# Kernel optimization log

Hardware: AMD Instinct MI355X
Metric: run time of the kernel (lower is better)

The kernel has to match this reference:

```python
import jax, jax.numpy as jnp
import numpy as np

B, S, D, H = 2, 2048, 512, 8


def setup_inputs() -> dict:
    key = jax.random.key(0)
    ks = jax.random.split(key, 9)
    scale = 1.0 / np.sqrt(D)
    x = jax.random.normal(ks[0], (B, S, D), dtype=jnp.float32)
    # Per-head full-width projections, stacked over heads: [H, D, D]
    Wq = jax.random.normal(ks[1], (H, D, D), dtype=jnp.float32) * scale
    Wk = jax.random.normal(ks[2], (H, D, D), dtype=jnp.float32) * scale
    Wv = jax.random.normal(ks[3], (H, D, D), dtype=jnp.float32) * scale
    bq = jax.random.normal(ks[4], (H, D), dtype=jnp.float32) * 0.01
    bk = jax.random.normal(ks[5], (H, D), dtype=jnp.float32) * 0.01
    bv = jax.random.normal(ks[6], (H, D), dtype=jnp.float32) * 0.01
    Wo = jax.random.normal(ks[7], (H * D, D), dtype=jnp.float32) * (1.0 / np.sqrt(H * D))
    bo = jax.random.normal(ks[8], (D,), dtype=jnp.float32) * 0.01
    return {"x": x, "Wq": Wq, "bq": bq, "Wk": Wk, "bk": bk, "Wv": Wv, "bv": bv, "Wo": Wo, "bo": bo}


def reference(x, Wq, bq, Wk, bk, Wv, bv, Wo, bo):
    # Batched per-head projections: [B,S,D] x [H,D,E] -> [B,H,S,E]
    q = jnp.einsum('bsd,hde->bhse', x, Wq) + bq[None, :, None, :]
    k = jnp.einsum('bsd,hde->bhse', x, Wk) + bk[None, :, None, :]
    v = jnp.einsum('bsd,hde->bhse', x, Wv) + bv[None, :, None, :]
    # NOTE: original module has NO 1/sqrt(d) scaling
    scores = jnp.einsum('bhse,bhte->bhst', q, k)  # [B,H,S,S]
    attn = jax.nn.softmax(scores, axis=-1)
    out = jnp.einsum('bhst,bhte->bhse', attn, v)  # [B,H,S,D]
    # Concat heads along feature dim: [B,S,H*D]
    cat = out.transpose(0, 2, 1, 3).reshape(B, S, H * D)
    return cat @ Wo + bo
```

## Files before the change

### kernel.cpp

```cpp
#include <hip/hip_runtime.h>

typedef _Float16 f16;
typedef _Float16 f16x8 __attribute__((ext_vector_type(8)));
typedef float f32x4 __attribute__((ext_vector_type(4)));

#define B_ 2
#define S_ 2048
#define D_ 512
#define H_ 8

__device__ inline void async_ld16(const void* g, void* l) {
  __builtin_amdgcn_global_load_lds((__attribute__((address_space(1))) void*)(g),
                                   (__attribute__((address_space(3))) void*)(l),
                                   16, 0, 0);
}

__global__ __launch_bounds__(256) void cvt_f16(const float* __restrict__ src,
                                               f16* __restrict__ dst, long n) {
  long i = (long)blockIdx.x * 256 + threadIdx.x;
  if (i >= n) return;
  dst[i] = (f16)src[i];
}

__global__ __launch_bounds__(256) void transpose_f32(const float* __restrict__ src,
                                                     f16* __restrict__ dst, int R, int C) {
  __shared__ float t[32][33];
  size_t zoff = (size_t)blockIdx.z * R * C;
  const float* s = src + zoff;
  int tx = threadIdx.x;
  int ty = threadIdx.y;
  int c0 = blockIdx.x * 32, r0 = blockIdx.y * 32;
#pragma unroll
  for (int i = 0; i < 4; ++i)
    t[ty + i * 8][tx] = s[(size_t)(r0 + ty + i * 8) * C + c0 + tx];
  __syncthreads();
#pragma unroll
  for (int i = 0; i < 4; ++i)
    dst[zoff + (size_t)(c0 + ty + i * 8) * R + r0 + tx] = (f16)t[tx][ty + i * 8];
}

__global__ __launch_bounds__(256) void reduce_out(const float* __restrict__ part,
                                                  const float* __restrict__ bo,
                                                  float* __restrict__ out, long n, int nslab) {
  long i = (long)blockIdx.x * 256 + threadIdx.x;
  if (i >= n) return;
  float v = bo[i & (D_ - 1)];
  for (int s = 0; s < nslab; ++s) v += part[(long)s * n + i];
  out[i] = v;
}

struct GemmArgs {
  const f16 *A, *Bm;
  void* C;
  const float* bias;
  float* Mloc;
  int K, lda, ldb, ldc;
  int zbase, NG, PBG;
  long sAp, sAb, sAg, sAz;
  long sBp, sBb, sBg, sBz;
  long sCp, sCb, sCg, sCz;
  long sbp, sbb, sbg, sbz;
  long sMlz;
};

template <typename OutT, int BIAS, bool PEXP>
__global__ __launch_bounds__(256) void gemm_nt(GemmArgs p) {
  int zloc = blockIdx.z;
  int zi = p.zbase + zloc;
  int pp = zi / p.PBG; int rz = zi - pp * p.PBG;
  int bb = rz / p.NG;  int g = rz - bb * p.NG;
  const f16* A  = p.A + (pp * p.sAp + bb * p.sAb + g * p.sAg + (long)zloc * p.sAz);
  const f16* Bm = p.Bm + (pp * p.sBp + bb * p.sBb + g * p.sBg + (long)zloc * p.sBz);
  OutT* C = (OutT*)p.C + (pp * p.sCp + bb * p.sCb + g * p.sCg + (long)zloc * p.sCz);
  const float* bias = nullptr;
  if (BIAS) bias = p.bias + (pp * p.sbp + bb * p.sbb + g * p.sbg + (long)zloc * p.sbz);

  __shared__ f16 lA[4096];
  __shared__ f16 lB[4096];
  __shared__ float lMx[PEXP ? 256 : 1];
  __shared__ f16 lR[PEXP ? 32 * 136 : 1];

  int tid = threadIdx.x;
  int lane = tid & 63;
  int w = tid >> 6;
  int wm = (w >> 1) << 6;
  int wn = (w & 1) << 6;
  long bm = (long)blockIdx.y * 128;
  long bn = (long)blockIdx.x * 128;

  f32x4 acc[4][4] = {};
  int qd = lane >> 4;
  int fr = lane & 15;

  int q0 = tid, q1 = tid + 256;
  int r0s = q0 >> 2, c0s = (q0 & 3) ^ ((r0s >> 1) & 3);
  int r1s = q1 >> 2, c1s = (q1 & 3) ^ ((r1s >> 1) & 3);

  for (int k0 = 0; k0 < p.K; k0 += 32) {
    long oa0 = (bm + r0s) * (long)p.lda + (k0 + c0s * 8);
    long oa1 = (bm + r1s) * (long)p.lda + (k0 + c1s * 8);
    long ob0 = (bn + r0s) * (long)p.ldb + (k0 + c0s * 8);
    long ob1 = (bn + r1s) * (long)p.ldb + (k0 + c1s * 8);
    __syncthreads();
    async_ld16(A + oa0,  lA + (size_t)q0 * 8);
    async_ld16(A + oa1,  lA + (size_t)q1 * 8);
    async_ld16(Bm + ob0, lB + (size_t)q0 * 8);
    async_ld16(Bm + ob1, lB + (size_t)q1 * 8);
    __syncthreads();

    f16x8 ah[4], bh[4];
#pragma unroll
    for (int i = 0; i < 4; ++i) {
      int m = wm + i * 16 + fr;
      ah[i] = *(const f16x8*)(lA + ((size_t)m * 4 + (qd ^ ((m >> 1) & 3))) * 8);
      int n = wn + i * 16 + fr;
      bh[i] = *(const f16x8*)(lB + ((size_t)n * 4 + (qd ^ ((n >> 1) & 3))) * 8);
    }
#pragma unroll
    for (int i = 0; i < 4; ++i)
#pragma unroll
      for (int j = 0; j < 4; ++j)
        acc[i][j] = __builtin_amdgcn_mfma_f32_16x16x32_f16(ah[i], bh[j], acc[i][j], 0, 0, 0);
  }

  int rr0 = qd * 4;
  if (PEXP) {
#pragma unroll
    for (int i = 0; i < 4; ++i) {
#pragma unroll
      for (int r = 0; r < 4; ++r) {
        float v = fmaxf(fmaxf(acc[i][0][r], acc[i][1][r]),
                        fmaxf(acc[i][2][r], acc[i][3][r]));
        v = fmaxf(v, __shfl_xor(v, 1, 64));
        v = fmaxf(v, __shfl_xor(v, 2, 64));
        v = fmaxf(v, __shfl_xor(v, 4, 64));
        v = fmaxf(v, __shfl_xor(v, 8, 64));
        if (fr == 0) lMx[(w & 1) * 128 + wm + i * 16 + rr0 + r] = v;
      }
    }
    __syncthreads();
    if (tid < 128) {
      float ml = fmaxf(lMx[tid], lMx[128 + tid]);
      p.Mloc[(long)zloc * p.sMlz + (long)blockIdx.x * S_ + bm + tid] = ml;
    }
    int rowBase = (w >> 1) << 4;
#pragma unroll
    for (int i = 0; i < 4; ++i) {
      __syncthreads();
#pragma unroll
      for (int r = 0; r < 4; ++r) {
        int rl = wm + i * 16 + rr0 + r;
        float ml = fmaxf(lMx[rl], lMx[128 + rl]);
        int rowLoc = rowBase + rr0 + r;
#pragma unroll
        for (int j = 0; j < 4; ++j) {
          int col = wn + j * 16 + fr;
          lR[rowLoc * 136 + col] = (f16)__expf(acc[i][j][r] - ml);
        }
      }
      __syncthreads();
      int rowLoc = tid >> 3;
      int colLoc = (tid & 7) * 16;
      long grow = bm + ((rowLoc & 15) + i * 16) + ((long)(rowLoc >> 4) << 6);
      f16x8 v0 = *(const f16x8*)(lR + rowLoc * 136 + colLoc);
      f16x8 v1 = *(const f16x8*)(lR + rowLoc * 136 + colLoc + 8);
      f16* dst = (f16*)C + grow * (long)p.ldc + bn + colLoc;
      *(f16x8*)(dst) = v0;
      *(f16x8*)(dst + 8) = v1;
    }
  } else {
#pragma unroll
    for (int i = 0; i < 4; ++i) {
#pragma unroll
      for (int j = 0; j < 4; ++j) {
#pragma unroll
        for (int r = 0; r < 4; ++r) {
          long row = bm + wm + i * 16 + rr0 + r;
          long col = bn + wn + j * 16 + fr;
          float v = acc[i][j][r];
          if (BIAS == 1) v += bias[col];
          if (BIAS == 2) v += bias[row];
          C[row * (long)p.ldc + col] = (OutT)v;
        }
      }
    }
  }
}

struct QkvArgs {
  const f16 *xh, *wqk, *wv;
  f16 *qk, *vT;
  const float *bqk, *bv;
};
__global__ __launch_bounds__(256) void qkv_proj(QkvArgs p) {
  const long SD = (long)S_ * D_, DD = (long)D_ * D_, DS = (long)D_ * S_;
  int zi = blockIdx.z;
  int pp = zi >> 4;
  int r = zi & 15;
  int b = r >> 3, h = r & 7;
  int bid = blockIdx.x;
  const f16 *A, *Bm;
  f16* C;
  const float* bias;
  long bm, bn;
  int ldc;
  bool biasRow;
  if (pp < 2) {
    A = p.xh + (long)b * SD;
    Bm = p.wqk + ((long)pp * 8 + h) * DD;
    C = p.qk + (long)zi * SD;
    bias = p.bqk + ((long)pp * 8 + h) * D_;
    bm = (long)(bid >> 2) * 128; bn = (long)(bid & 3) * 128;
    ldc = D_; biasRow = false;
  } else {
    A = p.wv + (long)h * DD;
    Bm = p.xh + (long)b * SD;
    C = p.vT + (long)(b * 8 + h) * DS;
    bias = p.bv + (long)h * D_;
    bm = (long)(bid >> 4) * 128; bn = (long)(bid & 15) * 128;
    ldc = S_; biasRow = true;
  }

  __shared__ f16 lA[4096];
  __shared__ f16 lB[4096];

  int tid = threadIdx.x;
  int lane = tid & 63;
  int w = tid >> 6;
  int wm = (w >> 1) << 6;
  int wn = (w & 1) << 6;

  f32x4 acc[4][4] = {};
  int qd = lane >> 4;
  int fr = lane & 15;

  int q0 = tid, q1 = tid + 256;
  int r0s = q0 >> 2, c0s = (q0 & 3) ^ ((r0s >> 1) & 3);
  int r1s = q1 >> 2, c1s = (q1 & 3) ^ ((r1s >> 1) & 3);

  for (int k0 = 0; k0 < D_; k0 += 32) {
    long oa0 = (bm + r0s) * (long)D_ + (k0 + c0s * 8);
    long oa1 = (bm + r1s) * (long)D_ + (k0 + c1s * 8);
    long ob0 = (bn + r0s) * (long)D_ + (k0 + c0s * 8);
    long ob1 = (bn + r1s) * (long)D_ + (k0 + c1s * 8);
    __syncthreads();
    async_ld16(A + oa0,  lA + (size_t)q0 * 8);
    async_ld16(A + oa1,  lA + (size_t)q1 * 8);
    async_ld16(Bm + ob0, lB + (size_t)q0 * 8);
    async_ld16(Bm + ob1, lB + (size_t)q1 * 8);
    __syncthreads();

    f16x8 ah[4], bh[4];
#pragma unroll
    for (int i = 0; i < 4; ++i) {
      int m = wm + i * 16 + fr;
      ah[i] = *(const f16x8*)(lA + ((size_t)m * 4 + (qd ^ ((m >> 1) & 3))) * 8);
      int n = wn + i * 16 + fr;
      bh[i] = *(const f16x8*)(lB + ((size_t)n * 4 + (qd ^ ((n >> 1) & 3))) * 8);
    }
#pragma unroll
    for (int i = 0; i < 4; ++i)
#pragma unroll
      for (int j = 0; j < 4; ++j)
        acc[i][j] = __builtin_amdgcn_mfma_f32_16x16x32_f16(ah[i], bh[j], acc[i][j], 0, 0, 0);
  }

  int rr0 = qd * 4;
#pragma unroll
  for (int i = 0; i < 4; ++i) {
#pragma unroll
    for (int j = 0; j < 4; ++j) {
#pragma unroll
      for (int r = 0; r < 4; ++r) {
        long row = bm + wm + i * 16 + rr0 + r;
        long col = bn + wn + j * 16 + fr;
        float v = acc[i][j][r] + (biasRow ? bias[row] : bias[col]);
        C[row * (long)ldc + col] = (f16)v;
      }
    }
  }
}

struct PvArgs {
  const f16* S; const float* Ml; const f16* V; f16* C;
  int ldc, zbase, NG;
  long sVz, sCb, sCg;
};
__global__ __launch_bounds__(256) void pv_flash(PvArgs p) {
  int zloc = blockIdx.z;
  int zi = p.zbase + zloc;
  int bb = zi / p.NG; int g = zi - bb * p.NG;
  const f16* Sm = p.S + (long)zloc * S_ * S_;
  const float* Ml = p.Ml + (long)zloc * 16 * S_;
  const f16* V = p.V + (long)zloc * p.sVz;
  f16* C = p.C + bb * p.sCb + g * p.sCg;

  __shared__ f16 lP[64 * 32];
  __shared__ f16 lV[128 * 32];

  int tid = threadIdx.x;
  int lane = tid & 63;
  int w = tid >> 6;
  long bm = (long)blockIdx.y * 64;
  long bn = (long)blockIdx.x * 128;
  int e0 = (w & 1) << 6;
  int m0 = (w >> 1) << 5;

  int qd = lane >> 4;
  int fr = lane & 15;

  f32x4 acc[2][4] = {};
  f32x4 lacc[2] = {};
  f16x8 ones;
#pragma unroll
  for (int j = 0; j < 8; ++j) ones[j] = (f16)1.0f;

  float mg[2];
#pragma unroll
  for (int i = 0; i < 2; ++i) {
    float m = -1e30f;
#pragma unroll
    for (int cb = 0; cb < 16; ++cb)
      m = fmaxf(m, Ml[cb * S_ + bm + m0 + i * 16 + fr]);
    mg[i] = m;
  }
  f16 al16[2];

  int rs = tid >> 2, cs = (tid & 3) ^ ((rs >> 1) & 3);

  for (int k0 = 0; k0 < S_; k0 += 32) {
    if ((k0 & 127) == 0) {
      int cb = k0 >> 7;
#pragma unroll
      for (int i = 0; i < 2; ++i)
        al16[i] = (f16)__expf(Ml[cb * S_ + bm + m0 + i * 16 + fr] - mg[i]);
    }
    __syncthreads();
    async_ld16(Sm + (bm + rs) * (long)S_ + (k0 + cs * 8), lP + (size_t)tid * 8);
#pragma unroll
    for (int j = 0; j < 2; ++j) {
      int q = j * 256 + tid;
      int rv = q >> 2, cv = (q & 3) ^ ((rv >> 1) & 3);
      async_ld16(V + (bn + rv) * (long)S_ + (k0 + cv * 8), lV + (size_t)q * 8);
    }
    __syncthreads();

    f16x8 ah[2], bh[4];
#pragma unroll
    for (int i = 0; i < 2; ++i) {
      int m = m0 + i * 16 + fr;
      ah[i] = *(const f16x8*)(lP + ((size_t)m * 4 + (qd ^ ((m >> 1) & 3))) * 8);
#pragma unroll
      for (int j = 0; j < 8; ++j) ah[i][j] *= al16[i];
    }
#pragma unroll
    for (int j = 0; j < 4; ++j) {
      int n = e0 + j * 16 + fr;
      bh[j] = *(const f16x8*)(lV + ((size_t)n * 4 + (qd ^ ((n >> 1) & 3))) * 8);
    }
#pragma unroll
    for (int i = 0; i < 2; ++i) {
      lacc[i] = __builtin_amdgcn_mfma_f32_16x16x32_f16(ah[i], ones, lacc[i], 0, 0, 0);
#pragma unroll
      for (int j = 0; j < 4; ++j)
        acc[i][j] = __builtin_amdgcn_mfma_f32_16x16x32_f16(ah[i], bh[j], acc[i][j], 0, 0, 0);
    }
  }

  int rr0 = qd * 4;
#pragma unroll
  for (int i = 0; i < 2; ++i) {
    float inv[4];
#pragma unroll
    for (int r = 0; r < 4; ++r) inv[r] = 1.0f / lacc[i][r];
#pragma unroll
    for (int j = 0; j < 4; ++j) {
#pragma unroll
      for (int r = 0; r < 4; ++r) {
        long row = bm + m0 + i * 16 + rr0 + r;
        long col = bn + e0 + j * 16 + fr;
        C[row * (long)p.ldc + col] = (f16)(acc[i][j][r] * inv[r]);
      }
    }
  }
}

extern "C" void kernel_launch(void* const* d_in, const int* in_sizes, int n_in,
                              void* d_out, int out_size, void* d_ws, size_t ws_size,
                              hipStream_t stream) {
  const float* x  = (const float*)d_in[0];
  const float* Wq = (const float*)d_in[1];
  const float* bq = (const float*)d_in[2];
  const float* Wk = (const float*)d_in[3];
  const float* bk = (const float*)d_in[4];
  const float* Wv = (const float*)d_in[5];
  const float* bv = (const float*)d_in[6];
  const float* Wo = (const float*)d_in[7];
  const float* bo = (const float*)d_in[8];
  float* out = (float*)d_out;

  auto al = [](size_t v) { return (v + 255) & ~(size_t)255; };
  const size_t eX = (size_t)B_ * S_ * D_;
  const size_t eW = (size_t)H_ * D_ * D_;
  const size_t eSS = (size_t)S_ * S_;
  const long SD = (long)S_ * D_;
  const long DD = (long)D_ * D_;
  const long DS = (long)D_ * S_;

  size_t fixed = al(eX * 2) + al(2 * eW * 2) + al(eW * 2) + al(eW * 2)
               + al(2ULL * H_ * D_ * 4);
  int NB = 1, GH = 1, GS = 1; bool found = false;
  for (int nb = 2; nb >= 1 && !found; --nb)
    for (int gh = 8; gh >= 1 && !found; gh >>= 1)
      for (int gs = nb * gh; gs >= 1 && !found; gs >>= 1) {
        size_t need = fixed + al((size_t)nb * S_ * H_ * D_ * 2)
                    + al(2ULL * nb * gh * S_ * D_ * 2)
                    + al((size_t)nb * gh * D_ * S_ * 2)
                    + al(4ULL * nb * SD * 4)
                    + al((size_t)gs * eSS * 2)
                    + al((size_t)gs * 16 * S_ * 4);
        if (need <= ws_size) { NB = nb; GH = gh; GS = gs; found = true; }
      }

  char* p0 = (char*)d_ws;
  size_t off = 0;
  f16* xh    = (f16*)(p0 + off); off += al(eX * 2);
  f16* wqk   = (f16*)(p0 + off); off += al(2 * eW * 2);
  f16* wv    = (f16*)(p0 + off); off += al(eW * 2);
  f16* wo    = (f16*)(p0 + off); off += al(eW * 2);
  float* bqk = (float*)(p0 + off); off += al(2ULL * H_ * D_ * 4);
  f16* catb  = (f16*)(p0 + off); off += al((size_t)NB * S_ * H_ * D_ * 2);
  f16* qk    = (f16*)(p0 + off); off += al(2ULL * NB * GH * S_ * D_ * 2);
  f16* vT    = (f16*)(p0 + off); off += al((size_t)NB * GH * D_ * S_ * 2);
  float* opart = (float*)(p0 + off); off += al(4ULL * NB * SD * 4);
  f16* scores = (f16*)(p0 + off); off += al((size_t)GS * eSS * 2);
  float* mloc = (float*)(p0 + off);

  cvt_f16<<<dim3((unsigned)((eX + 255) / 256)), 256, 0, stream>>>(x, xh, (long)eX);
  dim3 tb(32, 8, 1);
  transpose_f32<<<dim3(16, 16, H_), tb, 0, stream>>>(Wq, wqk, D_, D_);
  transpose_f32<<<dim3(16, 16, H_), tb, 0, stream>>>(Wk, wqk + eW, D_, D_);
  transpose_f32<<<dim3(16, 16, H_), tb, 0, stream>>>(Wv, wv, D_, D_);
  transpose_f32<<<dim3(16, 128, 1), tb, 0, stream>>>(Wo, wo, H_ * D_, D_);
  hipMemcpyAsync(bqk, bq, (size_t)H_ * D_ * 4, hipMemcpyDeviceToDevice, stream);
  hipMemcpyAsync(bqk + H_ * D_, bk, (size_t)H_ * D_ * 4, hipMemcpyDeviceToDevice, stream);

  for (int b0 = 0; b0 < B_; b0 += NB) {
    for (int h0 = 0; h0 < H_; h0 += GH) {
      if (NB == 2 && GH == 8) {
        QkvArgs a{xh, wqk, wv, qk, vT, bqk, bv};
        qkv_proj<<<dim3(64, 1, 48), 256, 0, stream>>>(a);
      } else {
        {
          GemmArgs a{};
          a.A = xh + (long)b0 * SD;
          a.Bm = wqk + (long)h0 * DD;
          a.C = qk; a.bias = bqk + (long)h0 * D_;
          a.K = D_; a.lda = D_; a.ldb = D_; a.ldc = D_;
          a.zbase = 0; a.NG = GH; a.PBG = NB * GH;
          a.sAb = SD;
          a.sBp = (long)H_ * DD; a.sBg = DD;
          a.sCz = SD;
          a.sbp = (long)H_ * D_; a.sbg = D_;
          gemm_nt<f16, 1, false><<<dim3(4, 16, 2 * NB * GH), 256, 0, stream>>>(a);
        }
        {
          GemmArgs a{};
          a.A = wv + (long)h0 * DD; a.Bm = xh + (long)b0 * SD;
          a.C = vT; a.bias = bv + (long)h0 * D_;
          a.K = D_; a.lda = D_; a.ldb = D_; a.ldc = S_;
          a.zbase = 0; a.NG = GH; a.PBG = NB * GH;
          a.sAg = DD;
          a.sBb = SD;
          a.sCz = DS;
          a.sbg = D_;
          gemm_nt<f16, 2, false><<<dim3(16, 4, NB * GH), 256, 0, stream>>>(a);
        }
      }
      for (int g0 = 0; g0 < NB * GH; g0 += GS) {
        {
          GemmArgs a{};
          a.A = qk + (long)g0 * SD;
          a.Bm = qk + ((long)NB * GH + g0) * SD;
          a.C = scores; a.Mloc = mloc;
          a.K = D_; a.lda = D_; a.ldb = D_; a.ldc = S_;
          a.zbase = g0; a.NG = GH; a.PBG = NB * GH;
          a.sAz = SD; a.sBz = SD; a.sCz = (long)eSS;
          a.sMlz = 16L * S_;
          gemm_nt<f16, 0, true><<<dim3(16, 16, GS), 256, 0, stream>>>(a);
        }
        {
          PvArgs a{};
          a.S = scores; a.Ml = mloc; a.V = vT + (long)g0 * DS;
          a.C = catb + (long)h0 * D_;
          a.ldc = H_ * D_; a.zbase = g0; a.NG = GH;
          a.sVz = DS; a.sCb = (long)S_ * H_ * D_; a.sCg = D_;
          pv_flash<<<dim3(4, S_ / 64, GS), 256, 0, stream>>>(a);
        }
      }
    }
    {
      GemmArgs a{};
      a.A = catb; a.Bm = wo;
      a.C = opart;
      a.K = 1024; a.lda = H_ * D_; a.ldb = H_ * D_; a.ldc = D_;
      a.zbase = 0; a.NG = 4; a.PBG = NB * 4;
      a.sAb = (long)S_ * H_ * D_; a.sAg = 1024;
      a.sBg = 1024;
      a.sCb = SD; a.sCg = (long)NB * SD;
      gemm_nt<float, 0, false><<<dim3(4, 16, NB * 4), 256, 0, stream>>>(a);
    }
    reduce_out<<<dim3((unsigned)(((long)NB * SD + 255) / 256)), 256, 0, stream>>>(
        opart, bo, out + (long)b0 * SD, (long)NB * SD, 4);
  }
}
```

Before: 498.2 us.

## Compute softmax row sums in score kernel; widen PV K-step to 64

The score GEMM now also accumulates per-block row sums of the exponentials, reduced by shuffles, and writes them next to the per-block maxima. The PV kernel rescales these partial sums with the global max instead of running an extra MFMA against a vector of ones to get the denominator. It also loads two 32-wide K tiles per barrier pair, which halves the number of syncs and doubles the LDS buffers. The trade-offs are extra shuffles and an extra global write in the score kernel, plus the row sums now come from fp32 exponentials rather than the fp16-rounded values that are actually multiplied with V.

```diff
diff --git a/kernel.cpp b/kernel.cpp
--- a/kernel.cpp
+++ b/kernel.cpp
@@ -54,6 +54,7 @@
   void* C;
   const float* bias;
   float* Mloc;
+  float* Lloc;
   int K, lda, ldb, ldc;
   int zbase, NG, PBG;
   long sAp, sAb, sAg, sAz;
@@ -78,6 +79,7 @@
   __shared__ f16 lA[4096];
   __shared__ f16 lB[4096];
   __shared__ float lMx[PEXP ? 256 : 1];
+  __shared__ float lSm[PEXP ? 256 : 1];
   __shared__ f16 lR[PEXP ? 32 * 136 : 1];
 
   int tid = threadIdx.x;
@@ -152,11 +154,19 @@
         int rl = wm + i * 16 + rr0 + r;
         float ml = fmaxf(lMx[rl], lMx[128 + rl]);
         int rowLoc = rowBase + rr0 + r;
+        float rsum = 0.f;
 #pragma unroll
         for (int j = 0; j < 4; ++j) {
           int col = wn + j * 16 + fr;
-          lR[rowLoc * 136 + col] = (f16)__expf(acc[i][j][r] - ml);
+          float e = __expf(acc[i][j][r] - ml);
+          rsum += e;
+          lR[rowLoc * 136 + col] = (f16)e;
         }
+        rsum += __shfl_xor(rsum, 1, 64);
+        rsum += __shfl_xor(rsum, 2, 64);
+        rsum += __shfl_xor(rsum, 4, 64);
+        rsum += __shfl_xor(rsum, 8, 64);
+        if (fr == 0) lSm[(w & 1) * 128 + rl] = rsum;
       }
       __syncthreads();
       int rowLoc = tid >> 3;
@@ -168,6 +178,10 @@
       *(f16x8*)(dst) = v0;
       *(f16x8*)(dst + 8) = v1;
     }
+    __syncthreads();
+    if (tid < 128)
+      p.Lloc[(long)zloc * p.sMlz + (long)blockIdx.x * S_ + bm + tid] =
+          lSm[tid] + lSm[128 + tid];
   } else {
 #pragma unroll
     for (int i = 0; i < 4; ++i) {
@@ -282,7 +296,7 @@
 }
 
 struct PvArgs {
-  const f16* S; const float* Ml; const f16* V; f16* C;
+  const f16* S; const float* Ml; const float* Ll; const f16* V; f16* C;
   int ldc, zbase, NG;
   long sVz, sCb, sCg;
 };
@@ -292,11 +306,12 @@
   int bb = zi / p.NG; int g = zi - bb * p.NG;
   const f16* Sm = p.S + (long)zloc * S_ * S_;
   const float* Ml = p.Ml + (long)zloc * 16 * S_;
+  const float* Ll = p.Ll + (long)zloc * 16 * S_;
   const f16* V = p.V + (long)zloc * p.sVz;
   f16* C = p.C + bb * p.sCb + g * p.sCg;
 
-  __shared__ f16 lP[64 * 32];
-  __shared__ f16 lV[128 * 32];
+  __shared__ f16 lP[2][64 * 32];
+  __shared__ f16 lV[2][128 * 32];
 
   int tid = threadIdx.x;
   int lane = tid & 63;
@@ -308,14 +323,11 @@
 
   int qd = lane >> 4;
   int fr = lane & 15;
+  int rr0 = qd * 4;
 
   f32x4 acc[2][4] = {};
-  f32x4 lacc[2] = {};
-  f16x8 ones;
-#pragma unroll
-  for (int j = 0; j < 8; ++j) ones[j] = (f16)1.0f;
-
-  float mg[2];
+
+  float mg[2], lsum[2];
 #pragma unroll
   for (int i = 0; i < 2; ++i) {
     float m = -1e30f;
@@ -323,12 +335,18 @@
     for (int cb = 0; cb < 16; ++cb)
       m = fmaxf(m, Ml[cb * S_ + bm + m0 + i * 16 + fr]);
     mg[i] = m;
+    float s = 0.f;
+#pragma unroll
+    for (int cb = 0; cb < 16; ++cb)
+      s += Ll[cb * S_ + bm + m0 + i * 16 + fr] *
+           __expf(Ml[cb * S_ + bm + m0 + i * 16 + fr] - m);
+    lsum[i] = s;
   }
   f16 al16[2];
 
   int rs = tid >> 2, cs = (tid & 3) ^ ((rs >> 1) & 3);
 
-  for (int k0 = 0; k0 < S_; k0 += 32) {
+  for (int k0 = 0; k0 < S_; k0 += 64) {
     if ((k0 & 127) == 0) {
       int cb = k0 >> 7;
 #pragma unroll
@@ -336,43 +354,49 @@
         al16[i] = (f16)__expf(Ml[cb * S_ + bm + m0 + i * 16 + fr] - mg[i]);
     }
     __syncthreads();
-    async_ld16(Sm + (bm + rs) * (long)S_ + (k0 + cs * 8), lP + (size_t)tid * 8);
-#pragma unroll
-    for (int j = 0; j < 2; ++j) {
-      int q = j * 256 + tid;
-      int rv = q >> 2, cv = (q & 3) ^ ((rv >> 1) & 3);
-      async_ld16(V + (bn + rv) * (long)S_ + (k0 + cv * 8), lV + (size_t)q * 8);
-    }
-    __syncthreads();
-
-    f16x8 ah[2], bh[4];
-#pragma unroll
-    for (int i = 0; i < 2; ++i) {
-      int m = m0 + i * 16 + fr;
-      ah[i] = *(const f16x8*)(lP + ((size_t)m * 4 + (qd ^ ((m >> 1) & 3))) * 8);
-#pragma unroll
-      for (int j = 0; j < 8; ++j) ah[i][j] *= al16[i];
-    }
-#pragma unroll
-    for (int j = 0; j < 4; ++j) {
-      int n = e0 + j * 16 + fr;
-      bh[j] = *(const f16x8*)(lV + ((size_t)n * 4 + (qd ^ ((n >> 1) & 3))) * 8);
-    }
-#pragma unroll
-    for (int i = 0; i < 2; ++i) {
-      lacc[i] = __builtin_amdgcn_mfma_f32_16x16x32_f16(ah[i], ones, lacc[i], 0, 0, 0);
-#pragma unroll
-      for (int j = 0; j < 4; ++j)
-        acc[i][j] = __builtin_amdgcn_mfma_f32_16x16x32_f16(ah[i], bh[j], acc[i][j], 0, 0, 0);
-    }
-  }
-
-  int rr0 = qd * 4;
+#pragma unroll
+    for (int t = 0; t < 2; ++t) {
+      async_ld16(Sm + (bm + rs) * (long)S_ + (k0 + t * 32 + cs * 8),
+                 lP[t] + (size_t)tid * 8);
+#pragma unroll
+      for (int j = 0; j < 2; ++j) {
+        int q = j * 256 + tid;
+        int rv = q >> 2, cv = (q & 3) ^ ((rv >> 1) & 3);
+        async_ld16(V + (bn + rv) * (long)S_ + (k0 + t * 32 + cv * 8),
+                   lV[t] + (size_t)q * 8);
+      }
+    }
+    __syncthreads();
+
+#pragma unroll
+    for (int t = 0; t < 2; ++t) {
+      f16x8 ah[2], bh[4];
+#pragma unroll
+      for (int i = 0; i < 2; ++i) {
+        int m = m0 + i * 16 + fr;
+        ah[i] = *(const f16x8*)(lP[t] + ((size_t)m * 4 + (qd ^ ((m >> 1) & 3))) * 8);
+#pragma unroll
+        for (int j = 0; j < 8; ++j) ah[i][j] *= al16[i];
+      }
+#pragma unroll
+      for (int j = 0; j < 4; ++j) {
+        int n = e0 + j * 16 + fr;
+        bh[j] = *(const f16x8*)(lV[t] + ((size_t)n * 4 + (qd ^ ((n >> 1) & 3))) * 8);
+      }
+#pragma unroll
+      for (int i = 0; i < 2; ++i)
+#pragma unroll
+        for (int j = 0; j < 4; ++j)
+          acc[i][j] = __builtin_amdgcn_mfma_f32_16x16x32_f16(ah[i], bh[j], acc[i][j], 0, 0, 0);
+    }
+  }
+
 #pragma unroll
   for (int i = 0; i < 2; ++i) {
     float inv[4];
 #pragma unroll
-    for (int r = 0; r < 4; ++r) inv[r] = 1.0f / lacc[i][r];
+    for (int r = 0; r < 4; ++r)
+      inv[r] = 1.0f / __shfl(lsum[i], (lane & 48) | (rr0 + r), 64);
 #pragma unroll
     for (int j = 0; j < 4; ++j) {
 #pragma unroll
@@ -418,7 +442,7 @@
                     + al((size_t)nb * gh * D_ * S_ * 2)
                     + al(4ULL * nb * SD * 4)
                     + al((size_t)gs * eSS * 2)
-                    + al((size_t)gs * 16 * S_ * 4);
+                    + 2 * al((size_t)gs * 16 * S_ * 4);
         if (need <= ws_size) { NB = nb; GH = gh; GS = gs; found = true; }
       }
 
@@ -434,7 +458,8 @@
   f16* vT    = (f16*)(p0 + off); off += al((size_t)NB * GH * D_ * S_ * 2);
   float* opart = (float*)(p0 + off); off += al(4ULL * NB * SD * 4);
   f16* scores = (f16*)(p0 + off); off += al((size_t)GS * eSS * 2);
-  float* mloc = (float*)(p0 + off);
+  float* mloc = (float*)(p0 + off); off += al((size_t)GS * 16 * S_ * 4);
+  float* lloc = (float*)(p0 + off);
 
   cvt_f16<<<dim3((unsigned)((eX + 255) / 256)), 256, 0, stream>>>(x, xh, (long)eX);
   dim3 tb(32, 8, 1);
@@ -482,7 +507,7 @@
           GemmArgs a{};
           a.A = qk + (long)g0 * SD;
           a.Bm = qk + ((long)NB * GH + g0) * SD;
-          a.C = scores; a.Mloc = mloc;
+          a.C = scores; a.Mloc = mloc; a.Lloc = lloc;
           a.K = D_; a.lda = D_; a.ldb = D_; a.ldc = S_;
           a.zbase = g0; a.NG = GH; a.PBG = NB * GH;
           a.sAz = SD; a.sBz = SD; a.sCz = (long)eSS;
@@ -491,7 +516,7 @@
         }
         {
           PvArgs a{};
-          a.S = scores; a.Ml = mloc; a.V = vT + (long)g0 * DS;
+          a.S = scores; a.Ml = mloc; a.Ll = lloc; a.V = vT + (long)g0 * DS;
           a.C = catb + (long)h0 * D_;
           a.ldc = H_ * D_; a.zbase = g0; a.NG = GH;
           a.sVz = DS; a.sCb = (long)S_ * H_ * D_; a.sCg = D_;
```

New measurement: 527.9 us. 1.06x slower.

## Stage projection epilogue through LDS and load two K-slices per PV iteration

Applied to the files above, without the earlier changes.

The projection GEMM epilogue now writes the accumulator tile into shared memory with a padded stride, then issues coalesced 16-byte vector stores per row instead of scattered 2-byte stores. The PV flash kernel now loads two 32-wide K slices per iteration into separate LDS buffers, which halves the number of barrier pairs and gives each sync more MFMA work. In exchange the PV kernel uses twice the LDS, which may reduce occupancy, and the epilogue adds extra barriers.

```diff
diff --git a/kernel.cpp b/kernel.cpp
--- a/kernel.cpp
+++ b/kernel.cpp
@@ -221,8 +221,9 @@
     ldc = S_; biasRow = true;
   }
 
-  __shared__ f16 lA[4096];
-  __shared__ f16 lB[4096];
+  __shared__ f16 lAB[8192];
+  f16* lA = lAB;
+  f16* lB = lAB + 4096;
 
   int tid = threadIdx.x;
   int lane = tid & 63;
@@ -266,18 +267,31 @@
   }
 
   int rr0 = qd * 4;
+  int rowBase = (w >> 1) << 4;
+  f16* lR = lAB;
 #pragma unroll
   for (int i = 0; i < 4; ++i) {
-#pragma unroll
-    for (int j = 0; j < 4; ++j) {
-#pragma unroll
-      for (int r = 0; r < 4; ++r) {
-        long row = bm + wm + i * 16 + rr0 + r;
+    __syncthreads();
+#pragma unroll
+    for (int r = 0; r < 4; ++r) {
+      int rowLoc = rowBase + rr0 + r;
+      long row = bm + wm + i * 16 + rr0 + r;
+#pragma unroll
+      for (int j = 0; j < 4; ++j) {
         long col = bn + wn + j * 16 + fr;
         float v = acc[i][j][r] + (biasRow ? bias[row] : bias[col]);
-        C[row * (long)ldc + col] = (f16)v;
-      }
-    }
+        lR[rowLoc * 136 + wn + j * 16 + fr] = (f16)v;
+      }
+    }
+    __syncthreads();
+    int rowLoc = tid >> 3;
+    int colLoc = (tid & 7) * 16;
+    long grow = bm + ((rowLoc & 15) + i * 16) + ((long)(rowLoc >> 4) << 6);
+    f16x8 v0 = *(const f16x8*)(lR + rowLoc * 136 + colLoc);
+    f16x8 v1 = *(const f16x8*)(lR + rowLoc * 136 + colLoc + 8);
+    f16* dst = C + grow * (long)ldc + bn + colLoc;
+    *(f16x8*)dst = v0;
+    *(f16x8*)(dst + 8) = v1;
   }
 }
 
@@ -295,8 +309,8 @@
   const f16* V = p.V + (long)zloc * p.sVz;
   f16* C = p.C + bb * p.sCb + g * p.sCg;
 
-  __shared__ f16 lP[64 * 32];
-  __shared__ f16 lV[128 * 32];
+  __shared__ f16 lP[2][64 * 32];
+  __shared__ f16 lV[2][128 * 32];
 
   int tid = threadIdx.x;
   int lane = tid & 63;
@@ -328,7 +342,7 @@
 
   int rs = tid >> 2, cs = (tid & 3) ^ ((rs >> 1) & 3);
 
-  for (int k0 = 0; k0 < S_; k0 += 32) {
+  for (int k0 = 0; k0 < S_; k0 += 64) {
     if ((k0 & 127) == 0) {
       int cb = k0 >> 7;
 #pragma unroll
@@ -336,34 +350,42 @@
         al16[i] = (f16)__expf(Ml[cb * S_ + bm + m0 + i * 16 + fr] - mg[i]);
     }
     __syncthreads();
-    async_ld16(Sm + (bm + rs) * (long)S_ + (k0 + cs * 8), lP + (size_t)tid * 8);
-#pragma unroll
-    for (int j = 0; j < 2; ++j) {
-      int q = j * 256 + tid;
-      int rv = q >> 2, cv = (q & 3) ^ ((rv >> 1) & 3);
-      async_ld16(V + (bn + rv) * (long)S_ + (k0 + cv * 8), lV + (size_t)q * 8);
-    }
-    __syncthreads();
-
-    f16x8 ah[2], bh[4];
-#pragma unroll
-    for (int i = 0; i < 2; ++i) {
-      int m = m0 + i * 16 + fr;
-      ah[i] = *(const f16x8*)(lP + ((size_t)m * 4 + (qd ^ ((m >> 1) & 3))) * 8);
-#pragma unroll
-      for (int j = 0; j < 8; ++j) ah[i][j] *= al16[i];
-    }
-#pragma unroll
-    for (int j = 0; j < 4; ++j) {
-      int n = e0 + j * 16 + fr;
-      bh[j] = *(const f16x8*)(lV + ((size_t)n * 4 + (qd ^ ((n >> 1) & 3))) * 8);
-    }
-#pragma unroll
-    for (int i = 0; i < 2; ++i) {
-      lacc[i] = __builtin_amdgcn_mfma_f32_16x16x32_f16(ah[i], ones, lacc[i], 0, 0, 0);
-#pragma unroll
-      for (int j = 0; j < 4; ++j)
-        acc[i][j] = __builtin_amdgcn_mfma_f32_16x16x32_f16(ah[i], bh[j], acc[i][j], 0, 0, 0);
+#pragma unroll
+    for (int t = 0; t < 2; ++t) {
+      async_ld16(Sm + (bm + rs) * (long)S_ + (k0 + t * 32 + cs * 8),
+                 lP[t] + (size_t)tid * 8);
+#pragma unroll
+      for (int j = 0; j < 2; ++j) {
+        int q = j * 256 + tid;
+        int rv = q >> 2, cv = (q & 3) ^ ((rv >> 1) & 3);
+        async_ld16(V + (bn + rv) * (long)S_ + (k0 + t * 32 + cv * 8),
+                   lV[t] + (size_t)q * 8);
+      }
+    }
+    __syncthreads();
+
+#pragma unroll
+    for (int t = 0; t < 2; ++t) {
+      f16x8 ah[2], bh[4];
+#pragma unroll
+      for (int i = 0; i < 2; ++i) {
+        int m = m0 + i * 16 + fr;
+        ah[i] = *(const f16x8*)(lP[t] + ((size_t)m * 4 + (qd ^ ((m >> 1) & 3))) * 8);
+#pragma unroll
+        for (int j = 0; j < 8; ++j) ah[i][j] *= al16[i];
+      }
+#pragma unroll
+      for (int j = 0; j < 4; ++j) {
+        int n = e0 + j * 16 + fr;
+        bh[j] = *(const f16x8*)(lV[t] + ((size_t)n * 4 + (qd ^ ((n >> 1) & 3))) * 8);
+      }
+#pragma unroll
+      for (int i = 0; i < 2; ++i) {
+        lacc[i] = __builtin_amdgcn_mfma_f32_16x16x32_f16(ah[i], ones, lacc[i], 0, 0, 0);
+#pragma unroll
+        for (int j = 0; j < 4; ++j)
+          acc[i][j] = __builtin_amdgcn_mfma_f32_16x16x32_f16(ah[i], bh[j], acc[i][j], 0, 0, 0);
+      }
     }
   }
 
```

Measured after the change: 479.2 us. 1.04x faster.
